# Kernel optimization log

Hardware: AMD Instinct MI355X
Metric: run time of the kernel (lower is better)

Reference implementation:

```python
import jax, jax.numpy as jnp
import numpy as np

COMMITMENT_COST = 0.25


def setup_inputs() -> dict:
    key = jax.random.key(0)
    k1, k2 = jax.random.split(key)
    # z_latents: [B, H, W, D] encoder output latents
    z_latents = jax.random.normal(k1, (128, 32, 32, 64), dtype=jnp.float32)
    # embeddings: [D, K] codebook, uniform init like tf.random_uniform_initializer (default [-0.05, 0.05])
    embeddings = jax.random.uniform(k2, (64, 1024), dtype=jnp.float32, minval=-0.05, maxval=0.05)
    return {"z_latents": z_latents, "embeddings": embeddings}


def reference(z_latents, embeddings):
    d, k = embeddings.shape
    flat = z_latents.reshape(-1, d)  # [N, D]
    # squared L2 distances to each codebook entry: [N, K]
    distances = (
        jnp.sum(flat * flat, axis=1, keepdims=True)
        - 2.0 * (flat @ embeddings)
        + jnp.sum(embeddings * embeddings, axis=0, keepdims=True)
    )
    # argmax(-d) == argmin(d) (both take first occurrence on ties)
    encoding_indices = jnp.argmin(distances, axis=1)  # [N]
    # one-hot @ embeddings.T is just a gather of codebook rows
    quantized = jnp.take(embeddings.T, encoding_indices, axis=0).reshape(z_latents.shape)
    commitment_loss = jnp.mean((jax.lax.stop_gradient(quantized) - z_latents) ** 2)
    embedding_loss = jnp.mean((jax.lax.stop_gradient(z_latents) - quantized) ** 2)
    vq_loss = embedding_loss + COMMITMENT_COST * commitment_loss
    # straight-through estimator
    quantized_st = z_latents + jax.lax.stop_gradient(quantized - z_latents)
    return quantized_st, vq_loss
```

## Files before the change

kernel.cpp:

```cpp
#include <hip/hip_runtime.h>

#pragma clang fp contract(off)

typedef __attribute__((ext_vector_type(8))) short short8;
typedef __attribute__((ext_vector_type(4))) float f32x4;

#define MARGIN 0.02f

static __device__ __forceinline__ unsigned short f2b(float f) {
    union { float f; unsigned u; } x; x.f = f;
    unsigned u = x.u;
    return (unsigned short)((u + 0x7FFFu + ((u >> 16) & 1u)) >> 16);
}

template <int ES>
static __device__ __forceinline__ float np_dist(
    const float* __restrict__ zr, const float* __restrict__ ecol,
    float zn, float en) {
    float c = 0.f;
    #pragma unroll
    for (int i = 0; i < 64; ++i) c = fmaf(zr[i], ecol[i * ES], c);
    float t = zn - 2.f * c;
    return t + en;
}

template <bool ET>
__global__ __launch_bounds__(256) void vq_prep(
    const float* __restrict__ E, float* __restrict__ enorm,
    float* __restrict__ Et, unsigned* __restrict__ EbW) {
    __shared__ float sT[64][65];
    const int tid = threadIdx.x;
    const int w = tid >> 6;
    const int m64 = tid & 63;
    const int c0 = blockIdx.x * 64;

    #pragma unroll
    for (int r = 0; r < 16; ++r) {
        const int row = r * 4 + w;
        sT[row][m64] = E[row * 1024 + c0 + m64];
    }
    __syncthreads();

    if (ET) {
        #pragma unroll
        for (int it = 0; it < 16; ++it) {
            const int e = it * 256 + tid;
            const int col = e >> 6, d = e & 63;
            Et[(c0 + col) * 64 + d] = sT[d][col];
        }
    }
    #pragma unroll
    for (int it = 0; it < 8; ++it) {
        const int w0 = it * 256 + tid;
        const int cl = w0 >> 9;
        const int s = (w0 >> 8) & 1;
        const int ll = (w0 >> 2) & 63;
        const int j = (w0 & 3) * 2;
        const int d = s * 32 + (ll >> 4) * 8 + j;
        const int col = cl * 16 + (ll & 15);
        const unsigned lo = f2b(sT[d][col]);
        const unsigned hi = f2b(sT[d + 1][col]);
        EbW[(blockIdx.x * 4 + cl) * 512 + (w0 & 511)] = lo | (hi << 16);
    }
    if (tid < 64) {
        float s2 = 0.f;
        #pragma unroll
        for (int d = 0; d < 64; ++d) {
            float v = sT[d][tid];
            s2 = fmaf(v, v, s2);
        }
        enorm[c0 + tid] = s2;
    }
}

template <int MODE>
__global__ __launch_bounds__(256, 4) void vq_main(
    const float* __restrict__ z, const float* __restrict__ E,
    const float* __restrict__ Et, const unsigned short* __restrict__ Eb,
    const float* __restrict__ enorm, float* __restrict__ out) {
    __shared__ unsigned short sB[2][8192];
    __shared__ float sEn[1024];
    __shared__ float sZn[128];
    __shared__ int sIdx[128];
    __shared__ float sRed[4];

    const int tid = threadIdx.x;
    const int w = tid >> 6;
    const int l = tid & 63;
    const int quad = l >> 4;
    const int m = l & 15;
    const int b = blockIdx.x;

    auto stage = [&](int t, int buf) {
        const unsigned short* gp = Eb + t * 8192 + w * 2048 + l * 8;
        unsigned short* lp = &sB[buf][w * 2048];
        #pragma unroll
        for (int i = 0; i < 4; ++i) {
            __builtin_amdgcn_global_load_lds(
                (const __attribute__((address_space(1))) void*)(gp + i * 512),
                (__attribute__((address_space(3))) void*)(lp + i * 512),
                16, 0, 0);
        }
    };

    if constexpr (MODE < 2) {
        stage(0, 0);
        stage(1, 1);
    }

    if constexpr (MODE < 2) {
        ((float4*)sEn)[tid] = ((const float4*)enorm)[tid];
    } else {
        #pragma unroll
        for (int i = 0; i < 4; ++i) {
            const int col = tid + i * 256;
            float s2 = 0.f;
            #pragma unroll
            for (int d = 0; d < 64; ++d) {
                float v = E[d * 1024 + col];
                s2 = fmaf(v, v, s2);
            }
            sEn[col] = s2;
        }
    }

    if (tid < 128) {
        const float* zr = z + (b * 128 + tid) * 64;
        float S[16];
        #pragma unroll
        for (int u = 0; u < 16; ++u) { float v = zr[u]; S[u] = v * v; }
        #pragma unroll
        for (int t = 1; t < 4; ++t)
            #pragma unroll
            for (int u = 0; u < 16; ++u) {
                float v = zr[16 * t + u];
                float sq = v * v;
                S[u] = S[u] + sq;
            }
        float R0 = (S[0] + S[4]) + (S[8] + S[12]);
        float R1 = (S[1] + S[5]) + (S[9] + S[13]);
        float R2 = (S[2] + S[6]) + (S[10] + S[14]);
        float R3 = (S[3] + S[7]) + (S[11] + S[15]);
        sZn[tid] = (R0 + R1) + (R2 + R3);
    }

    short8 a[2][2];
    #pragma unroll
    for (int rt = 0; rt < 2; ++rt) {
        const int rowl = w * 32 + rt * 16 + m;
        #pragma unroll
        for (int s = 0; s < 2; ++s) {
            const float* zp = z + (b * 128 + rowl) * 64 + s * 32 + quad * 8;
            union { float4 v; float f[4]; } u0, u1;
            u0.v = *(const float4*)zp;
            u1.v = *(const float4*)(zp + 4);
            short8 av;
            #pragma unroll
            for (int j = 0; j < 4; ++j) av[j] = (short)f2b(u0.f[j]);
            #pragma unroll
            for (int j = 0; j < 4; ++j) av[4 + j] = (short)f2b(u1.f[j]);
            a[rt][s] = av;
        }
    }

    float v1p[2][4], v2p[2][4];
    #pragma unroll
    for (int rt = 0; rt < 2; ++rt)
        #pragma unroll
        for (int r = 0; r < 4; ++r) { v1p[rt][r] = 3.4e38f; v2p[rt][r] = 3.4e38f; }

    if constexpr (MODE < 2) {
        asm volatile("s_waitcnt vmcnt(4) lgkmcnt(0)" ::: "memory");
        __builtin_amdgcn_sched_barrier(0);
        __builtin_amdgcn_s_barrier();

        for (int st = 0; st < 8; ++st) {
            const unsigned short* bufp = &sB[st & 1][l * 8];
            #pragma unroll
            for (int ct = 0; ct < 8; ++ct) {
                const int c = st * 8 + ct;
                short8 b0 = *(const short8*)(bufp + ct * 1024);
                short8 b1 = *(const short8*)(bufp + ct * 1024 + 512);
                f32x4 acc0 = {0.f, 0.f, 0.f, 0.f};
                f32x4 acc1 = {0.f, 0.f, 0.f, 0.f};
                acc0 = __builtin_amdgcn_mfma_f32_16x16x32_bf16(a[0][0], b0, acc0, 0, 0, 0);
                acc0 = __builtin_amdgcn_mfma_f32_16x16x32_bf16(a[0][1], b1, acc0, 0, 0, 0);
                acc1 = __builtin_amdgcn_mfma_f32_16x16x32_bf16(a[1][0], b0, acc1, 0, 0, 0);
                acc1 = __builtin_amdgcn_mfma_f32_16x16x32_bf16(a[1][1], b1, acc1, 0, 0, 0);
                const float en = sEn[c * 16 + m];
                #pragma unroll
                for (int r = 0; r < 4; ++r) {
                    float p0 = fmaf(-2.f, acc0[r], en);
                    p0 = __uint_as_float((__float_as_uint(p0) & 0xFFFFFFC0u) | (unsigned)c);
                    v2p[0][r] = __builtin_amdgcn_fmed3f(p0, v1p[0][r], v2p[0][r]);
                    v1p[0][r] = fminf(p0, v1p[0][r]);
                    float p1 = fmaf(-2.f, acc1[r], en);
                    p1 = __uint_as_float((__float_as_uint(p1) & 0xFFFFFFC0u) | (unsigned)c);
                    v2p[1][r] = __builtin_amdgcn_fmed3f(p1, v1p[1][r], v2p[1][r]);
                    v1p[1][r] = fminf(p1, v1p[1][r]);
                }
            }
            if (st == 7) break;
            __builtin_amdgcn_s_barrier();
            if (st < 6) {
                stage(st + 2, st & 1);
                asm volatile("s_waitcnt vmcnt(4)" ::: "memory");
            } else {
                asm volatile("s_waitcnt vmcnt(0)" ::: "memory");
            }
            __builtin_amdgcn_sched_barrier(0);
            __builtin_amdgcn_s_barrier();
        }
    } else {
        unsigned short* sB0 = &sB[0][0];
        __syncthreads();
        for (int st = 0; st < 8; ++st) {
            #pragma unroll
            for (int i = 0; i < 4; ++i) {
                const int u = tid + i * 256;
                const int d0 = (u & 31) * 2;
                const int cg = u >> 5;
                const float* e0 = E + d0 * 1024 + st * 128 + cg * 4;
                union { float4 v; float f[4]; } va, vb;
                va.v = *(const float4*)e0;
                vb.v = *(const float4*)(e0 + 1024);
                #pragma unroll
                for (int j = 0; j < 4; ++j) {
                    const int col = cg * 4 + j;
                    const unsigned lo = f2b(va.f[j]);
                    const unsigned hi = f2b(vb.f[j]);
                    const int gi = col * 8 + ((d0 >> 3) ^ (col & 7));
                    *(unsigned*)&sB0[gi * 8 + (d0 & 7)] = lo | (hi << 16);
                }
            }
            __syncthreads();
            #pragma unroll
            for (int ct = 0; ct < 8; ++ct) {
                const int c = st * 8 + ct;
                const int colb = (ct * 16 + m) * 8;
                short8 b0 = *(const short8*)&sB0[(colb + (quad ^ (m & 7))) * 8];
                short8 b1 = *(const short8*)&sB0[(colb + ((4 + quad) ^ (m & 7))) * 8];
                f32x4 acc0 = {0.f, 0.f, 0.f, 0.f};
                f32x4 acc1 = {0.f, 0.f, 0.f, 0.f};
                acc0 = __builtin_amdgcn_mfma_f32_16x16x32_bf16(a[0][0], b0, acc0, 0, 0, 0);
                acc0 = __builtin_amdgcn_mfma_f32_16x16x32_bf16(a[0][1], b1, acc0, 0, 0, 0);
                acc1 = __builtin_amdgcn_mfma_f32_16x16x32_bf16(a[1][0], b0, acc1, 0, 0, 0);
                acc1 = __builtin_amdgcn_mfma_f32_16x16x32_bf16(a[1][1], b1, acc1, 0, 0, 0);
                const float en = sEn[c * 16 + m];
                #pragma unroll
                for (int r = 0; r < 4; ++r) {
                    float p0 = fmaf(-2.f, acc0[r], en);
                    p0 = __uint_as_float((__float_as_uint(p0) & 0xFFFFFFC0u) | (unsigned)c);
                    v2p[0][r] = __builtin_amdgcn_fmed3f(p0, v1p[0][r], v2p[0][r]);
                    v1p[0][r] = fminf(p0, v1p[0][r]);
                    float p1 = fmaf(-2.f, acc1[r], en);
                    p1 = __uint_as_float((__float_as_uint(p1) & 0xFFFFFFC0u) | (unsigned)c);
                    v2p[1][r] = __builtin_amdgcn_fmed3f(p1, v1p[1][r], v2p[1][r]);
                    v1p[1][r] = fminf(p1, v1p[1][r]);
                }
            }
            __syncthreads();
        }
    }

    constexpr bool viaEt = (MODE == 0);
    float la = 0.f;
    #pragma unroll
    for (int rt = 0; rt < 2; ++rt) {
        #pragma unroll
        for (int r = 0; r < 4; ++r) {
            float pv1 = v1p[rt][r];
            float vb = pv1;
            #pragma unroll
            for (int mask = 1; mask <= 8; mask <<= 1)
                vb = fminf(vb, __shfl_xor(vb, mask));
            const int rowl = w * 32 + rt * 16 + quad * 4 + r;
            const float zn = sZn[rowl];
            const float* zr = z + (b * 128 + rowl) * 64;
            float d = 3.4e38f;
            int kk = 0x7fffffff;
            if (pv1 <= vb + MARGIN) {
                kk = (int)(__float_as_uint(pv1) & 63u) * 16 + m;
                d = viaEt ? np_dist<1>(zr, Et + kk * 64, zn, sEn[kk])
                          : np_dist<1024>(zr, E + kk, zn, sEn[kk]);
            }
            float pv2 = v2p[rt][r];
            if (pv2 <= vb + MARGIN) {
                int kc = (int)(__float_as_uint(pv2) & 63u) * 16 + m;
                float dd = viaEt ? np_dist<1>(zr, Et + kc * 64, zn, sEn[kc])
                                 : np_dist<1024>(zr, E + kc, zn, sEn[kc]);
                if (dd < d || (dd == d && kc < kk)) { d = dd; kk = kc; }
            }
            #pragma unroll
            for (int mask = 1; mask <= 8; mask <<= 1) {
                float d2 = __shfl_xor(d, mask);
                int c2 = __shfl_xor(kk, mask);
                bool take = (d2 < d) || (d2 == d && c2 < kk);
                d = take ? d2 : d;
                kk = take ? c2 : kk;
            }
            if (m == 0) {
                sIdx[rowl] = kk;
                la += d;
            }
        }
    }
    __syncthreads();

    {
        const int row_local = w * 32 + (l >> 1);
        const int half = l & 1;
        const int idx = sIdx[row_local];
        union { float s[32]; float4 f[8]; } tmp;
        if (viaEt) {
            const float4* src = (const float4*)(Et + idx * 64 + half * 32);
            #pragma unroll
            for (int q4 = 0; q4 < 8; ++q4) tmp.f[q4] = src[q4];
        } else {
            #pragma unroll
            for (int dd = 0; dd < 32; ++dd) tmp.s[dd] = E[(half * 32 + dd) * 1024 + idx];
        }
        float4* dst = (float4*)(out + (b * 128 + row_local) * 64 + half * 32);
        #pragma unroll
        for (int q4 = 0; q4 < 8; ++q4) dst[q4] = tmp.f[q4];
    }

    #pragma unroll
    for (int mask = 32; mask >= 1; mask >>= 1) la += __shfl_xor(la, mask);
    if (l == 0) sRed[w] = la;
    __syncthreads();

    if (tid == 0) {
        const float blocksum = sRed[0] + sRed[1] + sRed[2] + sRed[3];
        atomicAdd(out + 8388608, blocksum * (1.25f / 8388608.f));
    }
}

extern "C" void kernel_launch(void* const* d_in, const int* in_sizes, int n_in,
                              void* d_out, int out_size, void* d_ws, size_t ws_size,
                              hipStream_t stream) {
    const float* z = (const float*)d_in[0];
    const float* E = (const float*)d_in[1];
    float* out = (float*)d_out;

    char* ws = (char*)d_ws;
    float* enorm = (float*)(ws + 128);
    unsigned short* Eb = (unsigned short*)(ws + 8192);
    float* Et = (float*)(ws + 139264);

    if (ws_size >= (size_t)401408) {
        vq_prep<true><<<16, 256, 0, stream>>>(E, enorm, Et, (unsigned*)Eb);
        vq_main<0><<<1024, 256, 0, stream>>>(z, E, Et, Eb, enorm, out);
    } else if (ws_size >= (size_t)139264) {
        vq_prep<false><<<16, 256, 0, stream>>>(E, enorm, Et, (unsigned*)Eb);
        vq_main<1><<<1024, 256, 0, stream>>>(z, E, Et, Eb, enorm, out);
    } else {
        vq_main<2><<<1024, 256, 0, stream>>>(z, E, Et, Eb, enorm, out);
    }
}
```

Before: 146.3 us.

## Halve rows per block to 64 and double grid for higher occupancy

Each block now processes 64 latent rows with one 16-row MFMA tile per wave instead of two, staging the codebook in 16 half-size chunks. LDS use is halved by shrinking the staging buffer and aliasing the small scratch arrays onto it, and launch bounds target 8 blocks per CU with a 2048-block grid. This aims to raise occupancy and latency hiding, at the cost of half the reuse of each staged codebook fragment and twice the total codebook traffic from L2.

```diff
diff --git a/kernel.cpp b/kernel.cpp
--- a/kernel.cpp
+++ b/kernel.cpp
@@ -74,15 +74,16 @@
 }
 
 template <int MODE>
-__global__ __launch_bounds__(256, 4) void vq_main(
+__global__ __launch_bounds__(256, 8) void vq_main(
     const float* __restrict__ z, const float* __restrict__ E,
     const float* __restrict__ Et, const unsigned short* __restrict__ Eb,
     const float* __restrict__ enorm, float* __restrict__ out) {
-    __shared__ unsigned short sB[2][8192];
+    __shared__ unsigned short sB[2][4096];
     __shared__ float sEn[1024];
-    __shared__ float sZn[128];
-    __shared__ int sIdx[128];
-    __shared__ float sRed[4];
+
+    float* sZn = (float*)&sB[0][0];
+    int* sIdx = (int*)((char*)&sB[0][0] + 256);
+    float* sRed = (float*)((char*)&sB[0][0] + 512);
 
     const int tid = threadIdx.x;
     const int w = tid >> 6;
@@ -91,11 +92,11 @@
     const int m = l & 15;
     const int b = blockIdx.x;
 
-    auto stage = [&](int t, int buf) {
-        const unsigned short* gp = Eb + t * 8192 + w * 2048 + l * 8;
-        unsigned short* lp = &sB[buf][w * 2048];
-        #pragma unroll
-        for (int i = 0; i < 4; ++i) {
+    auto stage = [&](int h, int buf) {
+        const unsigned short* gp = Eb + h * 4096 + w * 1024 + l * 8;
+        unsigned short* lp = &sB[buf][w * 1024];
+        #pragma unroll
+        for (int i = 0; i < 2; ++i) {
             __builtin_amdgcn_global_load_lds(
                 (const __attribute__((address_space(1))) void*)(gp + i * 512),
                 (__attribute__((address_space(3))) void*)(lp + i * 512),
@@ -106,9 +107,6 @@
     if constexpr (MODE < 2) {
         stage(0, 0);
         stage(1, 1);
-    }
-
-    if constexpr (MODE < 2) {
         ((float4*)sEn)[tid] = ((const float4*)enorm)[tid];
     } else {
         #pragma unroll
@@ -124,8 +122,105 @@
         }
     }
 
-    if (tid < 128) {
-        const float* zr = z + (b * 128 + tid) * 64;
+    short8 a[2];
+    {
+        const int rowl = w * 16 + m;
+        #pragma unroll
+        for (int s = 0; s < 2; ++s) {
+            const float* zp = z + (b * 64 + rowl) * 64 + s * 32 + quad * 8;
+            union { float4 v; float f[4]; } u0, u1;
+            u0.v = *(const float4*)zp;
+            u1.v = *(const float4*)(zp + 4);
+            short8 av;
+            #pragma unroll
+            for (int j = 0; j < 4; ++j) av[j] = (short)f2b(u0.f[j]);
+            #pragma unroll
+            for (int j = 0; j < 4; ++j) av[4 + j] = (short)f2b(u1.f[j]);
+            a[s] = av;
+        }
+    }
+
+    float v1p[4], v2p[4];
+    #pragma unroll
+    for (int r = 0; r < 4; ++r) { v1p[r] = 3.4e38f; v2p[r] = 3.4e38f; }
+
+    if constexpr (MODE < 2) {
+        asm volatile("s_waitcnt vmcnt(2) lgkmcnt(0)" ::: "memory");
+        __builtin_amdgcn_sched_barrier(0);
+        __builtin_amdgcn_s_barrier();
+
+        for (int h = 0; h < 16; ++h) {
+            const unsigned short* bufp = &sB[h & 1][l * 8];
+            #pragma unroll
+            for (int ct = 0; ct < 4; ++ct) {
+                const int c = h * 4 + ct;
+                short8 b0 = *(const short8*)(bufp + ct * 1024);
+                short8 b1 = *(const short8*)(bufp + ct * 1024 + 512);
+                f32x4 acc = {0.f, 0.f, 0.f, 0.f};
+                acc = __builtin_amdgcn_mfma_f32_16x16x32_bf16(a[0], b0, acc, 0, 0, 0);
+                acc = __builtin_amdgcn_mfma_f32_16x16x32_bf16(a[1], b1, acc, 0, 0, 0);
+                const float en = sEn[c * 16 + m];
+                #pragma unroll
+                for (int r = 0; r < 4; ++r) {
+                    float p0 = fmaf(-2.f, acc[r], en);
+                    p0 = __uint_as_float((__float_as_uint(p0) & 0xFFFFFFC0u) | (unsigned)c);
+                    v2p[r] = __builtin_amdgcn_fmed3f(p0, v1p[r], v2p[r]);
+                    v1p[r] = fminf(p0, v1p[r]);
+                }
+            }
+            if (h == 15) break;
+            __builtin_amdgcn_s_barrier();
+            if (h < 14) {
+                stage(h + 2, h & 1);
+                asm volatile("s_waitcnt vmcnt(2)" ::: "memory");
+            } else {
+                asm volatile("s_waitcnt vmcnt(0)" ::: "memory");
+            }
+            __builtin_amdgcn_sched_barrier(0);
+            __builtin_amdgcn_s_barrier();
+        }
+    } else {
+        unsigned* sW = (unsigned*)&sB[0][0];
+        __syncthreads();
+        for (int h = 0; h < 16; ++h) {
+            #pragma unroll
+            for (int it = 0; it < 8; ++it) {
+                const int w0 = it * 256 + tid;
+                const int cl = w0 >> 9;
+                const int s = (w0 >> 8) & 1;
+                const int ll = (w0 >> 2) & 63;
+                const int j = (w0 & 3) * 2;
+                const int d = s * 32 + (ll >> 4) * 8 + j;
+                const int col = (h * 4 + cl) * 16 + (ll & 15);
+                const unsigned lo = f2b(E[d * 1024 + col]);
+                const unsigned hi = f2b(E[(d + 1) * 1024 + col]);
+                sW[w0] = lo | (hi << 16);
+            }
+            __syncthreads();
+            const unsigned short* bufp = &sB[0][l * 8];
+            #pragma unroll
+            for (int ct = 0; ct < 4; ++ct) {
+                const int c = h * 4 + ct;
+                short8 b0 = *(const short8*)(bufp + ct * 1024);
+                short8 b1 = *(const short8*)(bufp + ct * 1024 + 512);
+                f32x4 acc = {0.f, 0.f, 0.f, 0.f};
+                acc = __builtin_amdgcn_mfma_f32_16x16x32_bf16(a[0], b0, acc, 0, 0, 0);
+                acc = __builtin_amdgcn_mfma_f32_16x16x32_bf16(a[1], b1, acc, 0, 0, 0);
+                const float en = sEn[c * 16 + m];
+                #pragma unroll
+                for (int r = 0; r < 4; ++r) {
+                    float p0 = fmaf(-2.f, acc[r], en);
+                    p0 = __uint_as_float((__float_as_uint(p0) & 0xFFFFFFC0u) | (unsigned)c);
+                    v2p[r] = __builtin_amdgcn_fmed3f(p0, v1p[r], v2p[r]);
+                    v1p[r] = fminf(p0, v1p[r]);
+                }
+            }
+            __syncthreads();
+        }
+    }
+
+    if (tid < 64) {
+        const float* zr = z + (b * 64 + tid) * 64;
         float S[16];
         #pragma unroll
         for (int u = 0; u < 16; ++u) { float v = zr[u]; S[u] = v * v; }
@@ -143,186 +238,65 @@
         float R3 = (S[3] + S[7]) + (S[11] + S[15]);
         sZn[tid] = (R0 + R1) + (R2 + R3);
     }
-
-    short8 a[2][2];
-    #pragma unroll
-    for (int rt = 0; rt < 2; ++rt) {
-        const int rowl = w * 32 + rt * 16 + m;
-        #pragma unroll
-        for (int s = 0; s < 2; ++s) {
-            const float* zp = z + (b * 128 + rowl) * 64 + s * 32 + quad * 8;
-            union { float4 v; float f[4]; } u0, u1;
-            u0.v = *(const float4*)zp;
-            u1.v = *(const float4*)(zp + 4);
-            short8 av;
-            #pragma unroll
-            for (int j = 0; j < 4; ++j) av[j] = (short)f2b(u0.f[j]);
-            #pragma unroll
-            for (int j = 0; j < 4; ++j) av[4 + j] = (short)f2b(u1.f[j]);
-            a[rt][s] = av;
-        }
-    }
-
-    float v1p[2][4], v2p[2][4];
-    #pragma unroll
-    for (int rt = 0; rt < 2; ++rt)
-        #pragma unroll
-        for (int r = 0; r < 4; ++r) { v1p[rt][r] = 3.4e38f; v2p[rt][r] = 3.4e38f; }
-
-    if constexpr (MODE < 2) {
-        asm volatile("s_waitcnt vmcnt(4) lgkmcnt(0)" ::: "memory");
-        __builtin_amdgcn_sched_barrier(0);
-        __builtin_amdgcn_s_barrier();
-
-        for (int st = 0; st < 8; ++st) {
-            const unsigned short* bufp = &sB[st & 1][l * 8];
-            #pragma unroll
-            for (int ct = 0; ct < 8; ++ct) {
-                const int c = st * 8 + ct;
-                short8 b0 = *(const short8*)(bufp + ct * 1024);
-                short8 b1 = *(const short8*)(bufp + ct * 1024 + 512);
-                f32x4 acc0 = {0.f, 0.f, 0.f, 0.f};
-                f32x4 acc1 = {0.f, 0.f, 0.f, 0.f};
-                acc0 = __builtin_amdgcn_mfma_f32_16x16x32_bf16(a[0][0], b0, acc0, 0, 0, 0);
-                acc0 = __builtin_amdgcn_mfma_f32_16x16x32_bf16(a[0][1], b1, acc0, 0, 0, 0);
-                acc1 = __builtin_amdgcn_mfma_f32_16x16x32_bf16(a[1][0], b0, acc1, 0, 0, 0);
-                acc1 = __builtin_amdgcn_mfma_f32_16x16x32_bf16(a[1][1], b1, acc1, 0, 0, 0);
-                const float en = sEn[c * 16 + m];
-                #pragma unroll
-                for (int r = 0; r < 4; ++r) {
-                    float p0 = fmaf(-2.f, acc0[r], en);
-                    p0 = __uint_as_float((__float_as_uint(p0) & 0xFFFFFFC0u) | (unsigned)c);
-                    v2p[0][r] = __builtin_amdgcn_fmed3f(p0, v1p[0][r], v2p[0][r]);
-                    v1p[0][r] = fminf(p0, v1p[0][r]);
-                    float p1 = fmaf(-2.f, acc1[r], en);
-                    p1 = __uint_as_float((__float_as_uint(p1) & 0xFFFFFFC0u) | (unsigned)c);
-                    v2p[1][r] = __builtin_amdgcn_fmed3f(p1, v1p[1][r], v2p[1][r]);
-                    v1p[1][r] = fminf(p1, v1p[1][r]);
-                }
-            }
-            if (st == 7) break;
-            __builtin_amdgcn_s_barrier();
-            if (st < 6) {
-                stage(st + 2, st & 1);
-                asm volatile("s_waitcnt vmcnt(4)" ::: "memory");
-            } else {
-                asm volatile("s_waitcnt vmcnt(0)" ::: "memory");
-            }
-            __builtin_amdgcn_sched_barrier(0);
-            __builtin_amdgcn_s_barrier();
-        }
-    } else {
-        unsigned short* sB0 = &sB[0][0];
-        __syncthreads();
-        for (int st = 0; st < 8; ++st) {
-            #pragma unroll
-            for (int i = 0; i < 4; ++i) {
-                const int u = tid + i * 256;
-                const int d0 = (u & 31) * 2;
-                const int cg = u >> 5;
-                const float* e0 = E + d0 * 1024 + st * 128 + cg * 4;
-                union { float4 v; float f[4]; } va, vb;
-                va.v = *(const float4*)e0;
-                vb.v = *(const float4*)(e0 + 1024);
-                #pragma unroll
-                for (int j = 0; j < 4; ++j) {
-                    const int col = cg * 4 + j;
-                    const unsigned lo = f2b(va.f[j]);
-                    const unsigned hi = f2b(vb.f[j]);
-                    const int gi = col * 8 + ((d0 >> 3) ^ (col & 7));
-                    *(unsigned*)&sB0[gi * 8 + (d0 & 7)] = lo | (hi << 16);
-                }
-            }
-            __syncthreads();
-            #pragma unroll
-            for (int ct = 0; ct < 8; ++ct) {
-                const int c = st * 8 + ct;
-                const int colb = (ct * 16 + m) * 8;
-                short8 b0 = *(const short8*)&sB0[(colb + (quad ^ (m & 7))) * 8];
-                short8 b1 = *(const short8*)&sB0[(colb + ((4 + quad) ^ (m & 7))) * 8];
-                f32x4 acc0 = {0.f, 0.f, 0.f, 0.f};
-                f32x4 acc1 = {0.f, 0.f, 0.f, 0.f};
-                acc0 = __builtin_amdgcn_mfma_f32_16x16x32_bf16(a[0][0], b0, acc0, 0, 0, 0);
-                acc0 = __builtin_amdgcn_mfma_f32_16x16x32_bf16(a[0][1], b1, acc0, 0, 0, 0);
-                acc1 = __builtin_amdgcn_mfma_f32_16x16x32_bf16(a[1][0], b0, acc1, 0, 0, 0);
-                acc1 = __builtin_amdgcn_mfma_f32_16x16x32_bf16(a[1][1], b1, acc1, 0, 0, 0);
-                const float en = sEn[c * 16 + m];
-                #pragma unroll
-                for (int r = 0; r < 4; ++r) {
-                    float p0 = fmaf(-2.f, acc0[r], en);
-                    p0 = __uint_as_float((__float_as_uint(p0) & 0xFFFFFFC0u) | (unsigned)c);
-                    v2p[0][r] = __builtin_amdgcn_fmed3f(p0, v1p[0][r], v2p[0][r]);
-                    v1p[0][r] = fminf(p0, v1p[0][r]);
-                    float p1 = fmaf(-2.f, acc1[r], en);
-                    p1 = __uint_as_float((__float_as_uint(p1) & 0xFFFFFFC0u) | (unsigned)c);
-                    v2p[1][r] = __builtin_amdgcn_fmed3f(p1, v1p[1][r], v2p[1][r]);
-                    v1p[1][r] = fminf(p1, v1p[1][r]);
-                }
-            }
-            __syncthreads();
-        }
-    }
+    __syncthreads();
 
     constexpr bool viaEt = (MODE == 0);
     float la = 0.f;
     #pragma unroll
-    for (int rt = 0; rt < 2; ++rt) {
-        #pragma unroll
-        for (int r = 0; r < 4; ++r) {
-            float pv1 = v1p[rt][r];
-            float vb = pv1;
-            #pragma unroll
-            for (int mask = 1; mask <= 8; mask <<= 1)
-                vb = fminf(vb, __shfl_xor(vb, mask));
-            const int rowl = w * 32 + rt * 16 + quad * 4 + r;
-            const float zn = sZn[rowl];
-            const float* zr = z + (b * 128 + rowl) * 64;
-            float d = 3.4e38f;
-            int kk = 0x7fffffff;
-            if (pv1 <= vb + MARGIN) {
-                kk = (int)(__float_as_uint(pv1) & 63u) * 16 + m;
-                d = viaEt ? np_dist<1>(zr, Et + kk * 64, zn, sEn[kk])
-                          : np_dist<1024>(zr, E + kk, zn, sEn[kk]);
-            }
-            float pv2 = v2p[rt][r];
-            if (pv2 <= vb + MARGIN) {
-                int kc = (int)(__float_as_uint(pv2) & 63u) * 16 + m;
-                float dd = viaEt ? np_dist<1>(zr, Et + kc * 64, zn, sEn[kc])
-                                 : np_dist<1024>(zr, E + kc, zn, sEn[kc]);
-                if (dd < d || (dd == d && kc < kk)) { d = dd; kk = kc; }
-            }
-            #pragma unroll
-            for (int mask = 1; mask <= 8; mask <<= 1) {
-                float d2 = __shfl_xor(d, mask);
-                int c2 = __shfl_xor(kk, mask);
-                bool take = (d2 < d) || (d2 == d && c2 < kk);
-                d = take ? d2 : d;
-                kk = take ? c2 : kk;
-            }
-            if (m == 0) {
-                sIdx[rowl] = kk;
-                la += d;
-            }
+    for (int r = 0; r < 4; ++r) {
+        float pv1 = v1p[r];
+        float vb = pv1;
+        #pragma unroll
+        for (int mask = 1; mask <= 8; mask <<= 1)
+            vb = fminf(vb, __shfl_xor(vb, mask));
+        const int rowl = w * 16 + quad * 4 + r;
+        const float zn = sZn[rowl];
+        const float* zr = z + (b * 64 + rowl) * 64;
+        float d = 3.4e38f;
+        int kk = 0x7fffffff;
+        if (pv1 <= vb + MARGIN) {
+            kk = (int)(__float_as_uint(pv1) & 63u) * 16 + m;
+            d = viaEt ? np_dist<1>(zr, Et + kk * 64, zn, sEn[kk])
+                      : np_dist<1024>(zr, E + kk, zn, sEn[kk]);
+        }
+        float pv2 = v2p[r];
+        if (pv2 <= vb + MARGIN) {
+            int kc = (int)(__float_as_uint(pv2) & 63u) * 16 + m;
+            float dd = viaEt ? np_dist<1>(zr, Et + kc * 64, zn, sEn[kc])
+                             : np_dist<1024>(zr, E + kc, zn, sEn[kc]);
+            if (dd < d || (dd == d && kc < kk)) { d = dd; kk = kc; }
+        }
+        #pragma unroll
+        for (int mask = 1; mask <= 8; mask <<= 1) {
+            float d2 = __shfl_xor(d, mask);
+            int c2 = __shfl_xor(kk, mask);
+            bool take = (d2 < d) || (d2 == d && c2 < kk);
+            d = take ? d2 : d;
+            kk = take ? c2 : kk;
+        }
+        if (m == 0) {
+            sIdx[rowl] = kk;
+            la += d;
         }
     }
     __syncthreads();
 
     {
-        const int row_local = w * 32 + (l >> 1);
-        const int half = l & 1;
+        const int row_local = w * 16 + (l >> 2);
+        const int part = l & 3;
         const int idx = sIdx[row_local];
-        union { float s[32]; float4 f[8]; } tmp;
+        union { float s[16]; float4 f[4]; } tmp;
         if (viaEt) {
-            const float4* src = (const float4*)(Et + idx * 64 + half * 32);
-            #pragma unroll
-            for (int q4 = 0; q4 < 8; ++q4) tmp.f[q4] = src[q4];
+            const float4* src = (const float4*)(Et + idx * 64 + part * 16);
+            #pragma unroll
+            for (int q4 = 0; q4 < 4; ++q4) tmp.f[q4] = src[q4];
         } else {
             #pragma unroll
-            for (int dd = 0; dd < 32; ++dd) tmp.s[dd] = E[(half * 32 + dd) * 1024 + idx];
-        }
-        float4* dst = (float4*)(out + (b * 128 + row_local) * 64 + half * 32);
-        #pragma unroll
-        for (int q4 = 0; q4 < 8; ++q4) dst[q4] = tmp.f[q4];
+            for (int dd = 0; dd < 16; ++dd) tmp.s[dd] = E[(part * 16 + dd) * 1024 + idx];
+        }
+        float4* dst = (float4*)(out + (b * 64 + row_local) * 64 + part * 16);
+        #pragma unroll
+        for (int q4 = 0; q4 < 4; ++q4) dst[q4] = tmp.f[q4];
     }
 
     #pragma unroll
@@ -350,11 +324,11 @@
 
     if (ws_size >= (size_t)401408) {
         vq_prep<true><<<16, 256, 0, stream>>>(E, enorm, Et, (unsigned*)Eb);
-        vq_main<0><<<1024, 256, 0, stream>>>(z, E, Et, Eb, enorm, out);
+        vq_main<0><<<2048, 256, 0, stream>>>(z, E, Et, Eb, enorm, out);
     } else if (ws_size >= (size_t)139264) {
         vq_prep<false><<<16, 256, 0, stream>>>(E, enorm, Et, (unsigned*)Eb);
-        vq_main<1><<<1024, 256, 0, stream>>>(z, E, Et, Eb, enorm, out);
+        vq_main<1><<<2048, 256, 0, stream>>>(z, E, Et, Eb, enorm, out);
     } else {
-        vq_main<2><<<1024, 256, 0, stream>>>(z, E, Et, Eb, enorm, out);
-    }
-}
+        vq_main<2><<<2048, 256, 0, stream>>>(z, E, Et, Eb, enorm, out);
+    }
+}
```

After: 140.1 us. 4.3% less time.
